# Performance work log

Measured on AMD Instinct MI355X. Metric: run time of the kernel, lower is better.

The kernel has to match this reference:

```python
import jax, jax.numpy as jnp
import numpy as np

N, E, D, L = 50000, 250000, 300, 5
ATOM_V, BOND_V = 128, 16
BN_EPS = 1e-5


def setup_inputs() -> dict:
    key = jax.random.key(0)
    ks = jax.random.split(key, 16)
    inp = {
        'x': jax.random.randint(ks[0], (N, 9), 0, ATOM_V),
        'edge_index': jax.random.randint(ks[1], (2, E), 0, N),
        'edge_attr': jax.random.randint(ks[2], (E, 3), 0, BOND_V),
        # learned parameters
        'atom_emb': jax.random.normal(ks[3], (9, ATOM_V, D), jnp.float32) * 0.02,
        'bond_emb': jax.random.normal(ks[4], (L, 3, BOND_V, D), jnp.float32) * 0.02,
        'eps': jnp.zeros((L,), jnp.float32),
        'W1': jax.random.normal(ks[5], (L, D, 2 * D), jnp.float32) / np.sqrt(D),
        'b1': jnp.zeros((L, 2 * D), jnp.float32),
        'g1': jnp.ones((L, 2 * D), jnp.float32),
        'be1': jnp.zeros((L, 2 * D), jnp.float32),
        'W2': jax.random.normal(ks[6], (L, 2 * D, D), jnp.float32) / np.sqrt(2 * D),
        'b2': jnp.zeros((L, D), jnp.float32),
        'gamma': jnp.ones((L, D), jnp.float32),
        'beta': jnp.zeros((L, D), jnp.float32),
    }
    return inp


def _bn(h, g, b):
    m = h.mean(0)
    v = h.var(0)
    return (h - m) * jax.lax.rsqrt(v + BN_EPS) * g + b


def reference(x, edge_index, edge_attr, atom_emb, bond_emb, eps, W1, b1, g1, be1, W2, b2, gamma, beta):
    src, dst = edge_index[0], edge_index[1]
    # AtomEncoder: sum of per-column embeddings -> [N, D]
    h = atom_emb[jnp.arange(9)[:, None], x.T].sum(0)
    for l in range(L):
        # BondEncoder for this layer -> [E, D]
        e = bond_emb[l][jnp.arange(3)[:, None], edge_attr.T].sum(0)
        # GIN: gather -> relu message -> scatter-add
        msg = jax.nn.relu(h[src] + e)
        agg = jax.ops.segment_sum(msg, dst, num_segments=N)
        z = (1.0 + eps[l]) * h + agg
        # MLP: Linear -> BN -> ReLU -> Linear
        z = jax.nn.relu(_bn(z @ W1[l] + b1[l], g1[l], be1[l])) @ W2[l] + b2[l]
        # outer BatchNorm
        h = _bn(z, gamma[l], beta[l])
        if l < L - 1:
            h = jax.nn.relu(h)
    return h  # JK='last'
```

## Files before the change

### kernel.cpp

```cpp
#include <hip/hip_runtime.h>

#define N_NODES 50000
#define N_EDGES 250000
#define DIM 300
#define DIM2 600
#define NL 5
#define MPAD 50048
#define KP1 320
#define KP2 608
#define NP1 640
#define NP2 384
#define SCAN_BLOCKS 196
#define CT_STRIDE 136

typedef __attribute__((ext_vector_type(8))) _Float16 half8;
typedef __attribute__((ext_vector_type(2))) _Float16 half2v;
typedef __attribute__((ext_vector_type(8))) short short8;
typedef __attribute__((ext_vector_type(4))) float f32x4;
typedef unsigned short ushort;
typedef unsigned int uint;

#define AS1 __attribute__((address_space(1)))
#define AS3 __attribute__((address_space(3)))

#define BARRIER() do { \
    asm volatile("" ::: "memory"); \
    __builtin_amdgcn_s_barrier(); \
    asm volatile("" ::: "memory"); \
} while (0)

static __device__ __forceinline__ ushort f2h(float f) {
    _Float16 h = (_Float16)f;
    return __builtin_bit_cast(ushort, h);
}
static __device__ __forceinline__ float h2f(ushort s) {
    return (float)__builtin_bit_cast(_Float16, s);
}
static __device__ __forceinline__ uint pk2(float a, float b) {
    return (uint)f2h(a) | ((uint)f2h(b) << 16);
}
static __device__ __forceinline__ half2v u2h2(uint u) {
    return __builtin_bit_cast(half2v, u);
}

static __device__ __forceinline__ int xcd_swizzle(int o, int nwg) {
    int q = nwg >> 3, r = nwg & 7;
    int xcd = o & 7, idx = o >> 3;
    return (xcd < r ? xcd * (q + 1) : r * (q + 1) + (xcd - r) * q) + idx;
}

__global__ void atom_enc(const int* __restrict__ x, const float* __restrict__ emb,
                         ushort* __restrict__ h) {
    int idx = blockIdx.x * blockDim.x + threadIdx.x;
    const int PAIRS = DIM / 2;
    if (idx >= N_NODES * PAIRS) return;
    int n = idx / PAIRS, p = idx - n * PAIRS;
    const int* xr = x + n * 9;
    float s0 = 0.f, s1 = 0.f;
#pragma unroll
    for (int i = 0; i < 9; i++) {
        const float2 v = *(const float2*)(emb + (size_t)(i * 128 + xr[i]) * DIM + 2 * p);
        s0 += v.x; s1 += v.y;
    }
    ((uint*)h)[idx] = pk2(s0, s1);
}

__global__ void deg_count(const int* __restrict__ ei, int* __restrict__ deg) {
    int e = blockIdx.x * blockDim.x + threadIdx.x;
    if (e < N_EDGES) atomicAdd(&deg[ei[N_EDGES + e]], 1);
}

__global__ void block_sums(const int* __restrict__ deg, int* __restrict__ bsum) {
    __shared__ int red[256];
    int tid = threadIdx.x;
    int node = blockIdx.x * 256 + tid;
    red[tid] = (node < N_NODES) ? deg[node] : 0;
    __syncthreads();
    for (int off = 128; off > 0; off >>= 1) {
        if (tid < off) red[tid] += red[tid + off];
        __syncthreads();
    }
    if (tid == 0) bsum[blockIdx.x] = red[0];
}

__global__ void scan_bsums(int* __restrict__ bsum) {
    __shared__ int s[256];
    int tid = threadIdx.x;
    int orig = (tid < SCAN_BLOCKS) ? bsum[tid] : 0;
    s[tid] = orig;
    __syncthreads();
    for (int off = 1; off < 256; off <<= 1) {
        int v = (tid >= off) ? s[tid - off] : 0;
        __syncthreads();
        s[tid] += v;
        __syncthreads();
    }
    if (tid < SCAN_BLOCKS) bsum[tid] = s[tid] - orig;
}

__global__ void write_rowstart(const int* __restrict__ deg, const int* __restrict__ bsum,
                               int* __restrict__ rowstart, int* __restrict__ cursor) {
    __shared__ int s[256];
    int tid = threadIdx.x;
    int node = blockIdx.x * 256 + tid;
    int d = (node < N_NODES) ? deg[node] : 0;
    s[tid] = d;
    __syncthreads();
    for (int off = 1; off < 256; off <<= 1) {
        int v = (tid >= off) ? s[tid - off] : 0;
        __syncthreads();
        s[tid] += v;
        __syncthreads();
    }
    int excl = s[tid] - d + bsum[blockIdx.x];
    if (node < N_NODES) {
        rowstart[node] = excl;
        cursor[node] = excl;
    }
    if (blockIdx.x == 0 && tid == 0) rowstart[N_NODES] = N_EDGES;
}

__global__ void csr_fill(const int* __restrict__ ei, const int* __restrict__ ea,
                         int* __restrict__ cursor, int2* __restrict__ epack) {
    int e = blockIdx.x * blockDim.x + threadIdx.x;
    if (e < N_EDGES) {
        int d = ei[N_EDGES + e];
        int slot = atomicAdd(&cursor[d], 1);
        int attr = ea[3 * e] | (ea[3 * e + 1] << 8) | (ea[3 * e + 2] << 16);
        epack[slot] = make_int2(ei[e], attr);
    }
}

__global__ void bond_conv(const float* __restrict__ bond, ushort* __restrict__ bondh) {
    int idx = blockIdx.x * blockDim.x + threadIdx.x;
    if (idx >= 48 * (DIM / 2)) return;
    float2 v = *(const float2*)(bond + 2 * idx);
    ((uint*)bondh)[idx] = pk2(v.x, v.y);
}

__global__ void init_bn(float* __restrict__ scale, float* __restrict__ shift) {
    int i = blockIdx.x * blockDim.x + threadIdx.x;
    if (i < DIM) { scale[i] = 1.f; shift[i] = 0.f; }
}

__launch_bounds__(256)
__global__ void agg_combine(const int* __restrict__ rowstart, const int2* __restrict__ epack,
                            const ushort* __restrict__ bondh, const ushort* __restrict__ h,
                            const float* __restrict__ scale, const float* __restrict__ shift,
                            int relu, const float* __restrict__ epsp, int layer,
                            ushort* __restrict__ A1) {
    int node = blockIdx.x * 4 + (threadIdx.x >> 6);
    int lane = threadIdx.x & 63;
    if (node >= MPAD) return;
    uint* row32 = (uint*)(A1 + (size_t)node * KP1);
    if (node >= N_NODES) {
        for (int i = lane; i < KP1 / 2; i += 64) row32[i] = 0;
        return;
    }
    const int PAIRS = DIM / 2;
    float2 scf[3], shf[3];
    half2v sch[3], shh[3];
#pragma unroll
    for (int i = 0; i < 3; i++) {
        int p = lane + 64 * i;
        scf[i] = make_float2(0.f, 0.f);
        shf[i] = make_float2(0.f, 0.f);
        if (p < PAIRS) {
            scf[i] = *(const float2*)(scale + 2 * p);
            shf[i] = *(const float2*)(shift + 2 * p);
        }
        sch[i] = half2v{(_Float16)scf[i].x, (_Float16)scf[i].y};
        shh[i] = half2v{(_Float16)shf[i].x, (_Float16)shf[i].y};
    }
    float epsv = 1.0f + epsp[layer];
    const uint* hd = (const uint*)(h + (size_t)node * DIM);
    float ax[3], ay[3];
#pragma unroll
    for (int i = 0; i < 3; i++) {
        int p = lane + 64 * i;
        ax[i] = 0.f; ay[i] = 0.f;
        if (p < PAIRS) {
            uint u = hd[p];
            float vx = h2f((ushort)(u & 0xffffu)) * scf[i].x + shf[i].x;
            float vy = h2f((ushort)(u >> 16)) * scf[i].y + shf[i].y;
            if (relu) { vx = fmaxf(vx, 0.f); vy = fmaxf(vy, 0.f); }
            ax[i] = epsv * vx; ay[i] = epsv * vy;
        }
    }

    auto edge_contrib = [&](int2 pk) {
        const uint* hs = (const uint*)(h + (size_t)pk.x * DIM);
        int a0 = pk.y & 0xff, a1v = (pk.y >> 8) & 0xff, a2 = (pk.y >> 16) & 0xff;
        const uint* t0 = (const uint*)(bondh + a0 * DIM);
        const uint* t1 = (const uint*)(bondh + (16 + a1v) * DIM);
        const uint* t2 = (const uint*)(bondh + (32 + a2) * DIM);
        const half2v z = {};
#pragma unroll
        for (int i = 0; i < 3; i++) {
            int p = lane + 64 * i;
            if (p < PAIRS) {
                half2v hv = u2h2(hs[p]) * sch[i] + shh[i];
                if (relu) hv = __builtin_elementwise_max(hv, z);
                half2v m = hv + u2h2(t0[p]) + u2h2(t1[p]) + u2h2(t2[p]);
                m = __builtin_elementwise_max(m, z);
                ax[i] += (float)m.x;
                ay[i] += (float)m.y;
            }
        }
    };

    int e0 = rowstart[node], e1 = rowstart[node + 1];
    int t = e0;
    for (; t + 1 < e1; t += 2) {
        int2 p0 = epack[t];
        int2 p1 = epack[t + 1];
        edge_contrib(p0);
        edge_contrib(p1);
    }
    if (t < e1) edge_contrib(epack[t]);

#pragma unroll
    for (int i = 0; i < 3; i++) {
        int p = lane + 64 * i;
        if (p < KP1 / 2) row32[p] = (p < PAIRS) ? pk2(ax[i], ay[i]) : 0u;
    }
}

__global__ void wt_conv(const float* __restrict__ W, ushort* __restrict__ Wt,
                        int K, int Nc, int KP, int NP) {
    int idx = blockIdx.x * blockDim.x + threadIdx.x;
    if (idx >= KP * NP) return;
    int k = idx / NP, n = idx - k * NP;
    ushort v = 0;
    if (k < K && n < Nc) v = f2h(W[(size_t)k * Nc + n]);
    Wt[(size_t)n * KP + k] = v;
}

__global__ void wt_conv2(const float* __restrict__ W, const float* __restrict__ scale,
                         ushort* __restrict__ Wt) {
    int idx = blockIdx.x * blockDim.x + threadIdx.x;
    if (idx >= KP2 * NP2) return;
    int k = idx / NP2, n = idx - k * NP2;
    ushort v = 0;
    if (k < DIM2 && n < DIM) v = f2h(scale[k] * W[(size_t)k * DIM + n]);
    Wt[(size_t)n * KP2 + k] = v;
}

__launch_bounds__(256, 4)
__global__ void gemm_mfma(const ushort* __restrict__ A, const ushort* __restrict__ Wt,
                          const float* __restrict__ bias, ushort* __restrict__ Cout,
                          int M, int KP, int Nc, int strideC, int ntiles,
                          float* __restrict__ csum, float* __restrict__ csq) {
    __shared__ ushort smem[16384];
    __shared__ float s_sum[128], s_sq[128];

    int tid = threadIdx.x;
    int w = tid >> 6, lane = tid & 63;
    int quad = lane >> 4, lr = lane & 15;
    int wm = w >> 1, wn = w & 1;
    int wg = xcd_swizzle(blockIdx.x, gridDim.x);
    int m0 = (wg / ntiles) * 128;
    int n0 = (wg % ntiles) * 128;

    if (tid < 128) { s_sum[tid] = 0.f; s_sq[tid] = 0.f; }

    const int kchunk = ((lane & 3) ^ ((lane >> 3) & 3)) * 8;
    const int grow = lane >> 2;
    const ushort* Abase = A + (size_t)m0 * KP + kchunk;
    const ushort* Bbase = Wt + (size_t)n0 * KP + kchunk;
    const int xq = (quad ^ ((lr >> 1) & 3)) * 8;

    auto stage = [&](int k0, int buf) {
        ushort* dA = smem + buf * 8192;
#pragma unroll
        for (int c = w; c < 8; c += 4)
            __builtin_amdgcn_global_load_lds((const AS1 void*)(Abase + (size_t)(16 * c + grow) * KP + k0),
                                             (AS3 void*)(dA + c * 512), 16, 0, 0);
#pragma unroll
        for (int c = w; c < 8; c += 4)
            __builtin_amdgcn_global_load_lds((const AS1 void*)(Bbase + (size_t)(16 * c + grow) * KP + k0),
                                             (AS3 void*)(dA + 4096 + c * 512), 16, 0, 0);
    };

    f32x4 acc[4][4] = {};
    const int nk = KP >> 5;

    stage(0, 0);
    stage(32, 1);
    asm volatile("s_waitcnt vmcnt(4)" ::: "memory");
    BARRIER();

    for (int t = 0; t < nk; ++t) {
        const ushort* As = smem + (t & 1) * 8192;
        const ushort* Bs = As + 4096;
        half8 a[4], b[4];
#pragma unroll
        for (int mf = 0; mf < 4; mf++)
            a[mf] = __builtin_bit_cast(half8, *(const short8*)(As + (64 * wm + 16 * mf + lr) * 32 + xq));
#pragma unroll
        for (int nf = 0; nf < 4; nf++)
            b[nf] = __builtin_bit_cast(half8, *(const short8*)(Bs + (64 * wn + 16 * nf + lr) * 32 + xq));
        asm volatile("s_waitcnt lgkmcnt(0)" ::: "memory");
        BARRIER();

        if (t + 2 < nk) stage((t + 2) << 5, t & 1);

        __builtin_amdgcn_s_setprio(1);
#pragma unroll
        for (int mf = 0; mf < 4; mf++)
#pragma unroll
            for (int nf = 0; nf < 4; nf++)
                acc[mf][nf] = __builtin_amdgcn_mfma_f32_16x16x32_f16(a[mf], b[nf], acc[mf][nf], 0, 0, 0);
        __builtin_amdgcn_s_setprio(0);

        if (t + 2 < nk)       { asm volatile("s_waitcnt vmcnt(4)" ::: "memory"); }
        else if (t + 1 < nk)  { asm volatile("s_waitcnt vmcnt(0)" ::: "memory"); }
        BARRIER();
    }

#pragma unroll
    for (int half = 0; half < 2; half++) {
        if (wm == half) {
#pragma unroll
            for (int nf = 0; nf < 4; nf++) {
                int lcol = 64 * wn + 16 * nf + lr;
                int gn = n0 + lcol;
                float bv = (gn < Nc) ? bias[gn] : 0.f;
                float ps = 0.f, pq = 0.f;
#pragma unroll
                for (int mf = 0; mf < 4; mf++) {
#pragma unroll
                    for (int r = 0; r < 4; r++) {
                        int lrow = 16 * mf + quad * 4 + r;
                        float v = acc[mf][nf][r] + bv;
                        smem[lrow * CT_STRIDE + lcol] = f2h(v);
                        if (m0 + 64 * half + lrow < M && gn < Nc) { ps += v; pq += v * v; }
                    }
                }
                if (gn < Nc) {
                    atomicAdd(&s_sum[lcol], ps);
                    atomicAdd(&s_sq[lcol], pq);
                }
            }
        }
        __syncthreads();
#pragma unroll
        for (int it = 0; it < 4; it++) {
            int idx = tid + it * 256;
            int row = idx >> 4, ch = idx & 15;
            int gcol = n0 + ch * 8;
            if (gcol < strideC) {
                *(short8*)(Cout + (size_t)(m0 + 64 * half + row) * strideC + gcol) =
                    *(const short8*)(smem + row * CT_STRIDE + ch * 8);
            }
        }
        __syncthreads();
    }

    if (tid < 128) {
        int gn = n0 + tid;
        if (gn < Nc) {
            atomicAdd(&csum[gn], s_sum[tid]);
            atomicAdd(&csq[gn], s_sq[tid]);
        }
    }
}

__launch_bounds__(256)
__global__ void gemm2_fused(const ushort* __restrict__ yh, const ushort* __restrict__ Wt,
                            const ushort* __restrict__ t1h, const float* __restrict__ bias,
                            ushort* __restrict__ hout,
                            float* __restrict__ csum, float* __restrict__ csq) {
    __shared__ ushort smem[24576];
    __shared__ ushort s_t[KP2];
    __shared__ float s_sum[128], s_sq[128];

    int tid = threadIdx.x;
    int w = tid >> 6, lane = tid & 63;
    int quad = lane >> 4, lr = lane & 15;
    int wm = w >> 1, wn = w & 1;
    int wg = xcd_swizzle(blockIdx.x, gridDim.x);
    int m0 = (wg / 3) * 128;
    int n0 = (wg % 3) * 128;

    if (tid < 128) { s_sum[tid] = 0.f; s_sq[tid] = 0.f; }

    const int kchunk = ((lane & 3) ^ ((lane >> 3) & 3)) * 8;
    const int grow = lane >> 2;
    const ushort* Abase = yh + (size_t)m0 * KP2 + kchunk;
    const ushort* Bbase = Wt + (size_t)n0 * KP2 + kchunk;
    const int xq = (quad ^ ((lr >> 1) & 3)) * 8;

    auto stage = [&](int k0, int buf) {
        ushort* dA = smem + buf * 4096;
        ushort* dB = smem + 12288 + buf * 4096;
#pragma unroll
        for (int c = w; c < 8; c += 4)
            __builtin_amdgcn_global_load_lds((const AS1 void*)(Abase + (size_t)(16 * c + grow) * KP2 + k0),
                                             (AS3 void*)(dA + c * 512), 16, 0, 0);
#pragma unroll
        for (int c = w; c < 8; c += 4)
            __builtin_amdgcn_global_load_lds((const AS1 void*)(Bbase + (size_t)(16 * c + grow) * KP2 + k0),
                                             (AS3 void*)(dB + c * 512), 16, 0, 0);
    };

    for (int i = tid; i < KP2 / 2; i += 256) ((uint*)s_t)[i] = ((const uint*)t1h)[i];
    asm volatile("s_waitcnt vmcnt(0) lgkmcnt(0)" ::: "memory");
    stage(0, 0);
    stage(32, 1);
    asm volatile("s_waitcnt vmcnt(4)" ::: "memory");
    BARRIER();

    f32x4 acc[4][4] = {};
    const int nk = KP2 >> 5;

    int cur = 0;
    for (int t = 0; t < nk; ++t) {
        int s2 = cur + 2; if (s2 >= 3) s2 -= 3;
        if (t + 2 < nk) stage((t + 2) << 5, s2);

        const ushort* As = smem + cur * 4096;
        const ushort* Bs = smem + 12288 + cur * 4096;
        half8 a[4], b[4];
        half8 t8 = *(const half8*)(s_t + (t << 5) + quad * 8);
#pragma unroll
        for (int mf = 0; mf < 4; mf++)
            a[mf] = __builtin_bit_cast(half8, *(const short8*)(As + (64 * wm + 16 * mf + lr) * 32 + xq));
#pragma unroll
        for (int nf = 0; nf < 4; nf++)
            b[nf] = __builtin_bit_cast(half8, *(const short8*)(Bs + (64 * wn + 16 * nf + lr) * 32 + xq));
        asm volatile("s_waitcnt lgkmcnt(0)" ::: "memory");

        __builtin_amdgcn_s_setprio(1);
        {
            half8 z = {};
#pragma unroll
            for (int mf = 0; mf < 4; mf++)
                a[mf] = __builtin_elementwise_max(a[mf] + t8, z);
        }
#pragma unroll
        for (int mf = 0; mf < 4; mf++)
#pragma unroll
            for (int nf = 0; nf < 4; nf++)
                acc[mf][nf] = __builtin_amdgcn_mfma_f32_16x16x32_f16(a[mf], b[nf], acc[mf][nf], 0, 0, 0);
        __builtin_amdgcn_s_setprio(0);

        if (t + 2 < nk)       { asm volatile("s_waitcnt vmcnt(4)" ::: "memory"); }
        else if (t + 1 < nk)  { asm volatile("s_waitcnt vmcnt(0)" ::: "memory"); }
        BARRIER();

        cur = (cur + 1 == 3) ? 0 : cur + 1;
    }

#pragma unroll
    for (int half = 0; half < 2; half++) {
        if (wm == half) {
#pragma unroll
            for (int nf = 0; nf < 4; nf++) {
                int lcol = 64 * wn + 16 * nf + lr;
                int gn = n0 + lcol;
                float bv = (gn < DIM) ? bias[gn] : 0.f;
                float ps = 0.f, pq = 0.f;
#pragma unroll
                for (int mf = 0; mf < 4; mf++) {
#pragma unroll
                    for (int r = 0; r < 4; r++) {
                        int lrow = 16 * mf + quad * 4 + r;
                        float v = acc[mf][nf][r] + bv;
                        smem[lrow * CT_STRIDE + lcol] = f2h(v);
                        if (m0 + 64 * half + lrow < N_NODES && gn < DIM) { ps += v; pq += v * v; }
                    }
                }
                if (gn < DIM) {
                    atomicAdd(&s_sum[lcol], ps);
                    atomicAdd(&s_sq[lcol], pq);
                }
            }
        }
        __syncthreads();
#pragma unroll
        for (int it = 0; it < 8; it++) {
            int idx = tid + it * 256;
            int row = idx >> 5, ch = idx & 31;
            int gm = m0 + 64 * half + row, gcol = n0 + ch * 4;
            if (gm < N_NODES && gcol < DIM) {
                *(uint2*)(hout + (size_t)gm * DIM + gcol) =
                    *(const uint2*)(smem + row * CT_STRIDE + ch * 4);
            }
        }
        __syncthreads();
    }

    if (tid < 128) {
        int gn = n0 + tid;
        if (gn < DIM) {
            atomicAdd(&csum[gn], s_sum[tid]);
            atomicAdd(&csq[gn], s_sq[tid]);
        }
    }
}

__global__ void bn_finalize(const float* __restrict__ sum, const float* __restrict__ sq,
                            const float* __restrict__ g, const float* __restrict__ b,
                            float* __restrict__ scale, float* __restrict__ shift,
                            ushort* __restrict__ th, int n, int npad) {
    int i = blockIdx.x * blockDim.x + threadIdx.x;
    if (i >= n) {
        if (th && i < npad) th[i] = 0;
        return;
    }
    const float invN = 1.0f / (float)N_NODES;
    float m = sum[i] * invN;
    float v = sq[i] * invN - m * m;
    float inv = rsqrtf(v + 1e-5f);
    float sc = g[i] * inv;
    scale[i] = sc;
    shift[i] = b[i] - m * sc;
    if (th) th[i] = f2h((b[i] - m * sc) / sc);
}

__global__ void bn_apply_out(const ushort* __restrict__ h, const float* __restrict__ scale,
                             const float* __restrict__ shift, float* __restrict__ out) {
    int idx = blockIdx.x * blockDim.x + threadIdx.x;
    const int PAIRS = DIM / 2;
    if (idx >= N_NODES * PAIRS) return;
    int p = idx % PAIRS;
    uint u = ((const uint*)h)[idx];
    float2 sc = *(const float2*)(scale + 2 * p);
    float2 sh = *(const float2*)(shift + 2 * p);
    float2 o;
    o.x = h2f((ushort)(u & 0xffffu)) * sc.x + sh.x;
    o.y = h2f((ushort)(u >> 16)) * sc.y + sh.y;
    *(float2*)(out + 2 * idx) = o;
}

extern "C" void kernel_launch(void* const* d_in, const int* in_sizes, int n_in,
                              void* d_out, int out_size, void* d_ws, size_t ws_size,
                              hipStream_t stream) {
    const int* x = (const int*)d_in[0];
    const int* ei = (const int*)d_in[1];
    const int* ea = (const int*)d_in[2];
    const float* atom_emb = (const float*)d_in[3];
    const float* bond_emb = (const float*)d_in[4];
    const float* eps = (const float*)d_in[5];
    const float* W1 = (const float*)d_in[6];
    const float* b1 = (const float*)d_in[7];
    const float* g1 = (const float*)d_in[8];
    const float* be1 = (const float*)d_in[9];
    const float* W2 = (const float*)d_in[10];
    const float* b2 = (const float*)d_in[11];
    const float* gamma = (const float*)d_in[12];
    const float* beta = (const float*)d_in[13];
    float* out = (float*)d_out;

    float* ws = (float*)d_ws;
    ushort* h    = (ushort*)ws;
    ushort* A1h  = (ushort*)(ws + 7500000);
    ushort* yh   = (ushort*)(ws + 15507680);
    ushort* Wt1  = (ushort*)(ws + 30722272);
    ushort* Wt2  = (ushort*)(ws + 30824672);
    ushort* bondh = (ushort*)(ws + 30941408);
    float* stats = ws + 30948608;
    ushort* t1h  = (ushort*)(ws + 30952208);
    int* rowstart = (int*)(ws + 30952512);
    int* deg      = rowstart + 50001;
    int* cursor   = deg + 50000;
    int2* epack   = (int2*)(cursor + 50000 + 1);
    int* bsum     = (int*)(epack + 250000);

    float* sum1 = stats;
    float* sq1  = stats + 600;
    float* sum2 = stats + 1200;
    float* sq2  = stats + 1500;
    float* scale1 = stats + 1800;
    float* shift1 = stats + 2400;
    float* scale2 = stats + 3000;
    float* shift2 = stats + 3300;

    const int PAIRS_N = N_NODES * (DIM / 2);

    hipMemsetAsync(deg, 0, 50000 * sizeof(int), stream);
    deg_count<<<(N_EDGES + 255) / 256, 256, 0, stream>>>(ei, deg);
    block_sums<<<SCAN_BLOCKS, 256, 0, stream>>>(deg, bsum);
    scan_bsums<<<1, 256, 0, stream>>>(bsum);
    write_rowstart<<<SCAN_BLOCKS, 256, 0, stream>>>(deg, bsum, rowstart, cursor);
    csr_fill<<<(N_EDGES + 255) / 256, 256, 0, stream>>>(ei, ea, cursor, epack);

    atom_enc<<<(PAIRS_N + 255) / 256, 256, 0, stream>>>(x, atom_emb, h);
    init_bn<<<(DIM + 255) / 256, 256, 0, stream>>>(scale2, shift2);

    for (int l = 0; l < NL; ++l) {
        hipMemsetAsync(stats, 0, 1800 * sizeof(float), stream);

        bond_conv<<<(48 * (DIM / 2) + 255) / 256, 256, 0, stream>>>(
            bond_emb + (size_t)l * 3 * 16 * DIM, bondh);

        agg_combine<<<(MPAD + 3) / 4, 256, 0, stream>>>(rowstart, epack, bondh,
                                                        h, scale2, shift2, (l > 0) ? 1 : 0,
                                                        eps, l, A1h);

        wt_conv<<<(KP1 * NP1 + 255) / 256, 256, 0, stream>>>(W1 + (size_t)l * DIM * DIM2, Wt1,
                                                             DIM, DIM2, KP1, NP1);

        gemm_mfma<<<(MPAD / 128) * (NP1 / 128), 256, 0, stream>>>(
            A1h, Wt1, b1 + l * DIM2, yh, N_NODES, KP1, DIM2, KP2, NP1 / 128, sum1, sq1);

        bn_finalize<<<(KP2 + 255) / 256, 256, 0, stream>>>(sum1, sq1, g1 + l * DIM2,
                                                           be1 + l * DIM2, scale1, shift1,
                                                           t1h, DIM2, KP2);

        wt_conv2<<<(KP2 * NP2 + 255) / 256, 256, 0, stream>>>(W2 + (size_t)l * DIM2 * DIM,
                                                              scale1, Wt2);

        gemm2_fused<<<(MPAD / 128) * (NP2 / 128), 256, 0, stream>>>(
            yh, Wt2, t1h, b2 + l * DIM, h, sum2, sq2);

        bn_finalize<<<(DIM + 255) / 256, 256, 0, stream>>>(sum2, sq2, gamma + l * DIM,
                                                           beta + l * DIM, scale2, shift2,
                                                           nullptr, DIM, DIM);
    }

    bn_apply_out<<<(PAIRS_N + 255) / 256, 256, 0, stream>>>(h, scale2, shift2, out);
}
```

Measured before the change: 1.102 ms.

## Precompute BN+ReLU node features once per layer and fold BN finalize into consumers

Adds a pass that applies the outer BatchNorm and ReLU to h once per layer, writing a normalized half-precision copy (reusing the yh buffer). The gather kernel then reads pre-normalized rows instead of repeating scale/shift/relu for every edge. The bn_finalize kernels are removed: their statistics math is recomputed inside the weight-conversion and output kernels, and the bond and W1 conversions are merged into one launch. This trades an extra full pass over the node features for less per-edge arithmetic and fewer small launches.

```diff
diff --git a/kernel.cpp b/kernel.cpp
--- a/kernel.cpp
+++ b/kernel.cpp
@@ -131,23 +131,49 @@
     }
 }
 
-__global__ void bond_conv(const float* __restrict__ bond, ushort* __restrict__ bondh) {
+__global__ void bond_wt(const float* __restrict__ bond, ushort* __restrict__ bondh,
+                        const float* __restrict__ W, ushort* __restrict__ Wt) {
     int idx = blockIdx.x * blockDim.x + threadIdx.x;
-    if (idx >= 48 * (DIM / 2)) return;
-    float2 v = *(const float2*)(bond + 2 * idx);
-    ((uint*)bondh)[idx] = pk2(v.x, v.y);
-}
-
-__global__ void init_bn(float* __restrict__ scale, float* __restrict__ shift) {
-    int i = blockIdx.x * blockDim.x + threadIdx.x;
-    if (i < DIM) { scale[i] = 1.f; shift[i] = 0.f; }
+    const int NB = 48 * (DIM / 2);
+    if (idx < NB) {
+        float2 v = *(const float2*)(bond + 2 * idx);
+        ((uint*)bondh)[idx] = pk2(v.x, v.y);
+        return;
+    }
+    idx -= NB;
+    if (idx >= KP1 * NP1) return;
+    int k = idx / NP1, n = idx - k * NP1;
+    ushort v = 0;
+    if (k < DIM && n < DIM2) v = f2h(W[(size_t)k * DIM2 + n]);
+    Wt[(size_t)n * KP1 + k] = v;
+}
+
+__global__ void bn_relu_h(const ushort* __restrict__ h, const float* __restrict__ sum2,
+                          const float* __restrict__ sq2, const float* __restrict__ g,
+                          const float* __restrict__ b, ushort* __restrict__ ht) {
+    int idx = blockIdx.x * blockDim.x + threadIdx.x;
+    const int PAIRS = DIM / 2;
+    if (idx >= N_NODES * PAIRS) return;
+    int p = idx % PAIRS;
+    const float invN = 1.0f / (float)N_NODES;
+    float2 s = *(const float2*)(sum2 + 2 * p);
+    float2 q = *(const float2*)(sq2 + 2 * p);
+    float2 gv = *(const float2*)(g + 2 * p);
+    float2 bv = *(const float2*)(b + 2 * p);
+    float m0 = s.x * invN, m1 = s.y * invN;
+    float sc0 = gv.x * rsqrtf(q.x * invN - m0 * m0 + 1e-5f);
+    float sc1 = gv.y * rsqrtf(q.y * invN - m1 * m1 + 1e-5f);
+    float sh0 = bv.x - m0 * sc0, sh1 = bv.y - m1 * sc1;
+    uint u = ((const uint*)h)[idx];
+    float v0 = fmaxf(h2f((ushort)(u & 0xffffu)) * sc0 + sh0, 0.f);
+    float v1 = fmaxf(h2f((ushort)(u >> 16)) * sc1 + sh1, 0.f);
+    ((uint*)ht)[idx] = pk2(v0, v1);
 }
 
 __launch_bounds__(256)
 __global__ void agg_combine(const int* __restrict__ rowstart, const int2* __restrict__ epack,
-                            const ushort* __restrict__ bondh, const ushort* __restrict__ h,
-                            const float* __restrict__ scale, const float* __restrict__ shift,
-                            int relu, const float* __restrict__ epsp, int layer,
+                            const ushort* __restrict__ bondh, const ushort* __restrict__ ht,
+                            const float* __restrict__ epsp, int layer,
                             ushort* __restrict__ A1) {
     int node = blockIdx.x * 4 + (threadIdx.x >> 6);
     int lane = threadIdx.x & 63;
@@ -158,22 +184,8 @@
         return;
     }
     const int PAIRS = DIM / 2;
-    float2 scf[3], shf[3];
-    half2v sch[3], shh[3];
-#pragma unroll
-    for (int i = 0; i < 3; i++) {
-        int p = lane + 64 * i;
-        scf[i] = make_float2(0.f, 0.f);
-        shf[i] = make_float2(0.f, 0.f);
-        if (p < PAIRS) {
-            scf[i] = *(const float2*)(scale + 2 * p);
-            shf[i] = *(const float2*)(shift + 2 * p);
-        }
-        sch[i] = half2v{(_Float16)scf[i].x, (_Float16)scf[i].y};
-        shh[i] = half2v{(_Float16)shf[i].x, (_Float16)shf[i].y};
-    }
     float epsv = 1.0f + epsp[layer];
-    const uint* hd = (const uint*)(h + (size_t)node * DIM);
+    const uint* hd = (const uint*)(ht + (size_t)node * DIM);
     float ax[3], ay[3];
 #pragma unroll
     for (int i = 0; i < 3; i++) {
@@ -181,15 +193,13 @@
         ax[i] = 0.f; ay[i] = 0.f;
         if (p < PAIRS) {
             uint u = hd[p];
-            float vx = h2f((ushort)(u & 0xffffu)) * scf[i].x + shf[i].x;
-            float vy = h2f((ushort)(u >> 16)) * scf[i].y + shf[i].y;
-            if (relu) { vx = fmaxf(vx, 0.f); vy = fmaxf(vy, 0.f); }
-            ax[i] = epsv * vx; ay[i] = epsv * vy;
+            ax[i] = epsv * h2f((ushort)(u & 0xffffu));
+            ay[i] = epsv * h2f((ushort)(u >> 16));
         }
     }
 
     auto edge_contrib = [&](int2 pk) {
-        const uint* hs = (const uint*)(h + (size_t)pk.x * DIM);
+        const uint* hs = (const uint*)(ht + (size_t)pk.x * DIM);
         int a0 = pk.y & 0xff, a1v = (pk.y >> 8) & 0xff, a2 = (pk.y >> 16) & 0xff;
         const uint* t0 = (const uint*)(bondh + a0 * DIM);
         const uint* t1 = (const uint*)(bondh + (16 + a1v) * DIM);
@@ -199,9 +209,7 @@
         for (int i = 0; i < 3; i++) {
             int p = lane + 64 * i;
             if (p < PAIRS) {
-                half2v hv = u2h2(hs[p]) * sch[i] + shh[i];
-                if (relu) hv = __builtin_elementwise_max(hv, z);
-                half2v m = hv + u2h2(t0[p]) + u2h2(t1[p]) + u2h2(t2[p]);
+                half2v m = u2h2(hs[p]) + u2h2(t0[p]) + u2h2(t1[p]) + u2h2(t2[p]);
                 m = __builtin_elementwise_max(m, z);
                 ax[i] += (float)m.x;
                 ay[i] += (float)m.y;
@@ -226,23 +234,31 @@
     }
 }
 
-__global__ void wt_conv(const float* __restrict__ W, ushort* __restrict__ Wt,
-                        int K, int Nc, int KP, int NP) {
+__global__ void wt_conv2_bn1(const float* __restrict__ W, const float* __restrict__ sum1,
+                             const float* __restrict__ sq1, const float* __restrict__ g1v,
+                             const float* __restrict__ be1v, ushort* __restrict__ Wt,
+                             ushort* __restrict__ th) {
     int idx = blockIdx.x * blockDim.x + threadIdx.x;
-    if (idx >= KP * NP) return;
-    int k = idx / NP, n = idx - k * NP;
-    ushort v = 0;
-    if (k < K && n < Nc) v = f2h(W[(size_t)k * Nc + n]);
-    Wt[(size_t)n * KP + k] = v;
-}
-
-__global__ void wt_conv2(const float* __restrict__ W, const float* __restrict__ scale,
-                         ushort* __restrict__ Wt) {
-    int idx = blockIdx.x * blockDim.x + threadIdx.x;
+    const float invN = 1.0f / (float)N_NODES;
+    if (idx < KP2) {
+        ushort tv = 0;
+        if (idx < DIM2) {
+            float mean = sum1[idx] * invN;
+            float var = sq1[idx] * invN - mean * mean;
+            float sc = g1v[idx] * rsqrtf(var + 1e-5f);
+            tv = f2h(be1v[idx] / sc - mean);
+        }
+        th[idx] = tv;
+    }
     if (idx >= KP2 * NP2) return;
     int k = idx / NP2, n = idx - k * NP2;
     ushort v = 0;
-    if (k < DIM2 && n < DIM) v = f2h(scale[k] * W[(size_t)k * DIM + n]);
+    if (k < DIM2 && n < DIM) {
+        float mean = sum1[k] * invN;
+        float var = sq1[k] * invN - mean * mean;
+        float sc = g1v[k] * rsqrtf(var + 1e-5f);
+        v = f2h(sc * W[(size_t)k * DIM + n]);
+    }
     Wt[(size_t)n * KP2 + k] = v;
 }
 
@@ -500,37 +516,26 @@
     }
 }
 
-__global__ void bn_finalize(const float* __restrict__ sum, const float* __restrict__ sq,
-                            const float* __restrict__ g, const float* __restrict__ b,
-                            float* __restrict__ scale, float* __restrict__ shift,
-                            ushort* __restrict__ th, int n, int npad) {
-    int i = blockIdx.x * blockDim.x + threadIdx.x;
-    if (i >= n) {
-        if (th && i < npad) th[i] = 0;
-        return;
-    }
-    const float invN = 1.0f / (float)N_NODES;
-    float m = sum[i] * invN;
-    float v = sq[i] * invN - m * m;
-    float inv = rsqrtf(v + 1e-5f);
-    float sc = g[i] * inv;
-    scale[i] = sc;
-    shift[i] = b[i] - m * sc;
-    if (th) th[i] = f2h((b[i] - m * sc) / sc);
-}
-
-__global__ void bn_apply_out(const ushort* __restrict__ h, const float* __restrict__ scale,
-                             const float* __restrict__ shift, float* __restrict__ out) {
+__global__ void bn_apply_out(const ushort* __restrict__ h, const float* __restrict__ sum2,
+                             const float* __restrict__ sq2, const float* __restrict__ g,
+                             const float* __restrict__ b, float* __restrict__ out) {
     int idx = blockIdx.x * blockDim.x + threadIdx.x;
     const int PAIRS = DIM / 2;
     if (idx >= N_NODES * PAIRS) return;
     int p = idx % PAIRS;
+    const float invN = 1.0f / (float)N_NODES;
+    float2 s = *(const float2*)(sum2 + 2 * p);
+    float2 q = *(const float2*)(sq2 + 2 * p);
+    float2 gv = *(const float2*)(g + 2 * p);
+    float2 bv = *(const float2*)(b + 2 * p);
+    float m0 = s.x * invN, m1 = s.y * invN;
+    float sc0 = gv.x * rsqrtf(q.x * invN - m0 * m0 + 1e-5f);
+    float sc1 = gv.y * rsqrtf(q.y * invN - m1 * m1 + 1e-5f);
+    float sh0 = bv.x - m0 * sc0, sh1 = bv.y - m1 * sc1;
     uint u = ((const uint*)h)[idx];
-    float2 sc = *(const float2*)(scale + 2 * p);
-    float2 sh = *(const float2*)(shift + 2 * p);
     float2 o;
-    o.x = h2f((ushort)(u & 0xffffu)) * sc.x + sh.x;
-    o.y = h2f((ushort)(u >> 16)) * sc.y + sh.y;
+    o.x = h2f((ushort)(u & 0xffffu)) * sc0 + sh0;
+    o.y = h2f((ushort)(u >> 16)) * sc1 + sh1;
     *(float2*)(out + 2 * idx) = o;
 }
 
@@ -568,14 +573,12 @@
     int2* epack   = (int2*)(cursor + 50000 + 1);
     int* bsum     = (int*)(epack + 250000);
 
+    ushort* ht = yh;
+
     float* sum1 = stats;
     float* sq1  = stats + 600;
     float* sum2 = stats + 1200;
     float* sq2  = stats + 1500;
-    float* scale1 = stats + 1800;
-    float* shift1 = stats + 2400;
-    float* scale2 = stats + 3000;
-    float* shift2 = stats + 3300;
 
     const int PAIRS_N = N_NODES * (DIM / 2);
 
@@ -587,38 +590,32 @@
     csr_fill<<<(N_EDGES + 255) / 256, 256, 0, stream>>>(ei, ea, cursor, epack);
 
     atom_enc<<<(PAIRS_N + 255) / 256, 256, 0, stream>>>(x, atom_emb, h);
-    init_bn<<<(DIM + 255) / 256, 256, 0, stream>>>(scale2, shift2);
+
+    const int NBWT = 48 * (DIM / 2) + KP1 * NP1;
 
     for (int l = 0; l < NL; ++l) {
+        if (l > 0)
+            bn_relu_h<<<(PAIRS_N + 255) / 256, 256, 0, stream>>>(
+                h, sum2, sq2, gamma + (size_t)(l - 1) * DIM, beta + (size_t)(l - 1) * DIM, ht);
+
         hipMemsetAsync(stats, 0, 1800 * sizeof(float), stream);
 
-        bond_conv<<<(48 * (DIM / 2) + 255) / 256, 256, 0, stream>>>(
-            bond_emb + (size_t)l * 3 * 16 * DIM, bondh);
+        bond_wt<<<(NBWT + 255) / 256, 256, 0, stream>>>(
+            bond_emb + (size_t)l * 3 * 16 * DIM, bondh, W1 + (size_t)l * DIM * DIM2, Wt1);
 
         agg_combine<<<(MPAD + 3) / 4, 256, 0, stream>>>(rowstart, epack, bondh,
-                                                        h, scale2, shift2, (l > 0) ? 1 : 0,
-                                                        eps, l, A1h);
-
-        wt_conv<<<(KP1 * NP1 + 255) / 256, 256, 0, stream>>>(W1 + (size_t)l * DIM * DIM2, Wt1,
-                                                             DIM, DIM2, KP1, NP1);
+                                                        (l == 0) ? h : ht, eps, l, A1h);
 
         gemm_mfma<<<(MPAD / 128) * (NP1 / 128), 256, 0, stream>>>(
             A1h, Wt1, b1 + l * DIM2, yh, N_NODES, KP1, DIM2, KP2, NP1 / 128, sum1, sq1);
 
-        bn_finalize<<<(KP2 + 255) / 256, 256, 0, stream>>>(sum1, sq1, g1 + l * DIM2,
-                                                           be1 + l * DIM2, scale1, shift1,
-                                                           t1h, DIM2, KP2);
-
-        wt_conv2<<<(KP2 * NP2 + 255) / 256, 256, 0, stream>>>(W2 + (size_t)l * DIM2 * DIM,
-                                                              scale1, Wt2);
+        wt_conv2_bn1<<<(KP2 * NP2 + 255) / 256, 256, 0, stream>>>(
+            W2 + (size_t)l * DIM2 * DIM, sum1, sq1, g1 + l * DIM2, be1 + l * DIM2, Wt2, t1h);
 
         gemm2_fused<<<(MPAD / 128) * (NP2 / 128), 256, 0, stream>>>(
             yh, Wt2, t1h, b2 + l * DIM, h, sum2, sq2);
-
-        bn_finalize<<<(DIM + 255) / 256, 256, 0, stream>>>(sum2, sq2, gamma + l * DIM,
-                                                           beta + l * DIM, scale2, shift2,
-                                                           nullptr, DIM, DIM);
-    }
-
-    bn_apply_out<<<(PAIRS_N + 255) / 256, 256, 0, stream>>>(h, scale2, shift2, out);
-}
+    }
+
+    bn_apply_out<<<(PAIRS_N + 255) / 256, 256, 0, stream>>>(
+        h, sum2, sq2, gamma + (size_t)(NL - 1) * DIM, beta + (size_t)(NL - 1) * DIM, out);
+}
```

New measurement: 1.110 ms. Within noise of the previous version (+0.8%).
